# Kernel tuning notes

Hardware: AMD Instinct MI355X
Metric: run time of the kernel (lower is better)

The kernel has to match this reference:

```python
import jax, jax.numpy as jnp
import numpy as np

C_IN, D_STATE, EXPAND, KS = 64, 16, 2, 3
D_INNER = EXPAND * C_IN
HP_KS, HP_SIGMA = 15, 3.0
B, H, W = 4, 256, 256


def _gauss2d(ks, sigma):
    ax = jnp.arange(ks, dtype=jnp.float32) - (ks - 1) / 2.0
    g = jnp.exp(-(ax ** 2) / (2.0 * sigma ** 2))
    g = g / g.sum()
    return jnp.outer(g, g)


def _dwconv(x, w, pad):
    # x: [B,d,H,W], w: [d,1,kh,kw] depthwise
    return jax.lax.conv_general_dilated(
        x, w, window_strides=(1, 1), padding=[(pad, pad), (pad, pad)],
        dimension_numbers=("NCHW", "OIHW", "NCHW"),
        feature_group_count=x.shape[1])


def _selective_scan(u, dt, Bm, Cm, A, D, scan_axis):
    # u, dt: [B,d,H,W]; Bm, Cm: [B,N,H,W]; scan over scan_axis (2 or 3)
    u_s = jnp.moveaxis(u, scan_axis, 0)    # [L,B,d,M]
    dt_s = jnp.moveaxis(dt, scan_axis, 0)
    B_s = jnp.moveaxis(Bm, scan_axis, 0)   # [L,B,N,M]
    C_s = jnp.moveaxis(Cm, scan_axis, 0)
    Bb, d = u.shape[0], u.shape[1]
    M = u_s.shape[-1]
    N = A.shape[1]

    def step(h, inp):
        uj, dtj, Bj, Cj = inp                     # [B,d,M], [B,d,M], [B,N,M], [B,N,M]
        expA = jnp.exp(dtj[..., None] * A[None, :, None, :])   # [B,d,M,N]
        Bt = jnp.transpose(Bj, (0, 2, 1))[:, None]              # [B,1,M,N]
        Ct = jnp.transpose(Cj, (0, 2, 1))[:, None]
        h = expA * h + (uj * dtj)[..., None] * Bt               # [B,d,M,N]
        y = jnp.sum(h * Ct, axis=-1) + D[None, :, None] * uj    # [B,d,M]
        return h, y

    h0 = jnp.zeros((Bb, d, M, N), u.dtype)
    _, ys = jax.lax.scan(step, h0, (u_s, dt_s, B_s, C_s))
    return jnp.moveaxis(ys, 0, scan_axis)


def setup_inputs() -> dict:
    key = jax.random.key(0)
    ks = jax.random.split(key, 12)
    d, N = D_INNER, D_STATE
    A_log = -(jnp.linspace(0.0, 1.0, N, dtype=jnp.float32) * jnp.log(10.0))
    A_log = jnp.broadcast_to(A_log[None, :], (d, N)).astype(jnp.float32)
    return {
        "x": jax.random.normal(ks[0], (B, C_IN, H, W), jnp.float32),
        "in_proj_w": jax.random.normal(ks[1], (2 * d, C_IN), jnp.float32) * 0.05,
        "in_proj_b": jnp.zeros((2 * d,), jnp.float32),
        "dw_w": jax.random.normal(ks[2], (d, 1, KS, KS), jnp.float32) * 0.2,
        "dw_b": jnp.zeros((d,), jnp.float32),
        "xproj_w": jax.random.normal(ks[3], (1 + 2 * N, d), jnp.float32) * 0.05,
        "dtproj_w": jax.random.normal(ks[4], (d, 1), jnp.float32) * 0.5,
        "dtproj_b": jax.random.normal(ks[5], (d,), jnp.float32) * 0.5 - 4.0,
        "A_log": A_log,
        "D": jnp.ones((d,), jnp.float32),
        "out_w": jax.random.normal(ks[6], (C_IN, d), jnp.float32) * 0.05,
        "out_b": jnp.zeros((C_IN,), jnp.float32),
    }


def reference(x, in_proj_w, in_proj_b, dw_w, dw_b, xproj_w,
              dtproj_w, dtproj_b, A_log, D, out_w, out_b):
    d, N = D_INNER, D_STATE
    # in_proj (1x1 conv)
    uz = jnp.einsum("bchw,oc->bohw", x, in_proj_w) + in_proj_b[None, :, None, None]
    U, Z = uz[:, :d], uz[:, d:]
    # depthwise conv
    Uc = _dwconv(U, dw_w, KS // 2) + dw_b[None, :, None, None]
    # tanh(alpha * x) * weight + bias with alpha=0.5, weight=1, bias=0
    Uc = jnp.tanh(0.5 * Uc)
    # Gaussian high-pass: x - depthwise gaussian blur
    g = _gauss2d(HP_KS, HP_SIGMA)
    gk = jnp.broadcast_to(g[None, None], (d, 1, HP_KS, HP_KS))
    Uc = Uc - _dwconv(Uc, gk, HP_KS // 2)
    # x_proj (1x1 conv, no bias)
    params = jnp.einsum("bchw,oc->bohw", Uc, xproj_w)
    delta_in = params[:, :1]                 # [B,1,H,W]
    B_map = params[:, 1:1 + N]               # [B,N,H,W]
    C_map = params[:, 1 + N:1 + 2 * N]
    dt = jax.nn.softplus(jnp.einsum("bohw,do->bdhw", delta_in, dtproj_w)
                         + dtproj_b[None, :, None, None])
    A = -jnp.exp(A_log)
    Y_h = _selective_scan(Uc, dt, B_map, C_map, A, D, scan_axis=3)   # scan over W
    Y_v = _selective_scan(Y_h, dt, B_map, C_map, A, D, scan_axis=2)  # scan over H
    out = Y_v * jax.nn.sigmoid(Z)
    return jnp.einsum("bdhw,cd->bchw", out, out_w) + out_b[None, :, None, None]
```

## Files before the change

kernel.cpp:

```cpp
#include <hip/hip_runtime.h>
#include <hip/hip_bf16.h>
#include <math.h>

#define BB 4
#define CIN 64
#define DI 128
#define NS 16
#define HH 256
#define WW 256
#define HW 65536
#define NCH_P 33

__device__ __forceinline__ float softplusf(float x) {
    return fmaxf(x, 0.f) + __logf(1.0f + __expf(-fabsf(x)));
}
__device__ __forceinline__ float tanh_half(float a) {
    return 1.0f - 2.0f / (1.0f + __expf(a));
}
__device__ __forceinline__ float sigmoidf(float z) {
    return 1.0f / (1.0f + __expf(-z));
}

__device__ __forceinline__ void gauss15(float* g) {
    float s = 0.f;
#pragma unroll
    for (int i = 0; i < 15; ++i) {
        float a = (float)i - 7.0f;
        g[i] = __expf(-a * a / 18.0f);
        s += g[i];
    }
    float inv = 1.0f / s;
#pragma unroll
    for (int i = 0; i < 15; ++i) g[i] *= inv;
}

__global__ __launch_bounds__(256) void k_inproj(
    const float* __restrict__ xb, const float* __restrict__ w,
    const float* __restrict__ bias, float* __restrict__ Ub) {
    int p = blockIdx.x * 256 + threadIdx.x;
    int og = blockIdx.y * 64;
    float xv[CIN];
#pragma unroll
    for (int c = 0; c < CIN; ++c) xv[c] = xb[(size_t)c * HW + p];
#pragma unroll 2
    for (int o = og; o < og + 64; ++o) {
        float a0 = bias[o], a1 = 0.f, a2 = 0.f, a3 = 0.f;
        const float* wr = w + o * CIN;
#pragma unroll
        for (int c = 0; c < CIN; c += 4) {
            a0 = fmaf(xv[c],     wr[c],     a0);
            a1 = fmaf(xv[c + 1], wr[c + 1], a1);
            a2 = fmaf(xv[c + 2], wr[c + 2], a2);
            a3 = fmaf(xv[c + 3], wr[c + 3], a3);
        }
        Ub[(size_t)o * HW + p] = (a0 + a1) + (a2 + a3);
    }
}

#define TILE_H 16
__global__ __launch_bounds__(256) void k_conv(
    const float* __restrict__ Ub, const float* __restrict__ dww,
    const float* __restrict__ dwb, float* __restrict__ Ucb) {
    __shared__ float sU[32 * 256];
    __shared__ float sC[30 * 272];
    int c  = blockIdx.x >> 4;
    int t  = blockIdx.x & 15;
    int h0 = t * TILE_H;
    int w  = threadIdx.x;

    const float* base = Ub + (size_t)c * HW;
#pragma unroll
    for (int i = 0; i < 32; ++i) {
        int hh = h0 + i - 8;
        sU[i * 256 + w] = (hh >= 0 && hh < HH) ? base[hh * WW + w] : 0.f;
    }
    __syncthreads();

    float wt[9];
#pragma unroll
    for (int i = 0; i < 9; ++i) wt[i] = dww[c * 9 + i];
    float bb = dwb[c];

#pragma unroll
    for (int i = 0; i < 30; ++i) {
        int r = h0 + i - 7;
        float v = 0.f;
        if (r >= 0 && r < HH) {
            float acc = bb;
#pragma unroll
            for (int ky = 0; ky < 3; ++ky) {
                const float* ur = sU + (i + ky) * 256;
#pragma unroll
                for (int kx = 0; kx < 3; ++kx) {
                    int ww = w + kx - 1;
                    if (ww >= 0 && ww < WW) acc = fmaf(ur[ww], wt[ky * 3 + kx], acc);
                }
            }
            v = tanh_half(acc);
        }
        sC[i * 272 + w + 7] = v;
    }
    if (w < 7) {
#pragma unroll
        for (int i = 0; i < 30; ++i) { sC[i * 272 + w] = 0.f; sC[i * 272 + w + 263] = 0.f; }
    }
    __syncthreads();

    float g[15]; gauss15(g);
#pragma unroll
    for (int i = 0; i < 30; ++i) {
        float acc = 0.f;
#pragma unroll
        for (int k = 0; k < 15; ++k) acc = fmaf(sC[i * 272 + w + k], g[k], acc);
        sU[i * 256 + w] = acc;
    }
    float* outp = Ucb + (size_t)c * HW + h0 * WW + w;
#pragma unroll
    for (int i = 0; i < TILE_H; ++i) {
        float acc = 0.f;
#pragma unroll
        for (int k = 0; k < 15; ++k) acc = fmaf(sU[(i + k) * 256 + w], g[k], acc);
        float center = sC[(i + 7) * 272 + w + 7];
        outp[i * WW] = center - acc;
    }
}

__global__ __launch_bounds__(256) void k_xproj(
    const float* __restrict__ Uc, const float* __restrict__ xw,
    float* __restrict__ P) {
    int p = blockIdx.x * 256 + threadIdx.x;
    int b = p >> 16;
    int rem = p & 65535;
    const float* up = Uc + (size_t)b * DI * HW + rem;
    float acc[NCH_P];
#pragma unroll
    for (int o = 0; o < NCH_P; ++o) acc[o] = 0.f;
    for (int c = 0; c < DI; ++c) {
        float u = up[(size_t)c * HW];
#pragma unroll
        for (int o = 0; o < NCH_P; ++o) acc[o] = fmaf(u, xw[o * DI + c], acc[o]);
    }
    float* pp = P + (size_t)b * NCH_P * HW + rem;
#pragma unroll
    for (int o = 0; o < NCH_P; ++o) pp[(size_t)o * HW] = acc[o];
}

#define CW 32
__global__ __launch_bounds__(128) void k_scan_w(
    float* __restrict__ UY, const float* __restrict__ P,
    const float* __restrict__ A_log, const float* __restrict__ dtw,
    const float* __restrict__ dtb, const float* __restrict__ Dv) {
    __shared__ float sU[DI * 33];
    __shared__ float sP[CW * 36];
    int bh = blockIdx.x;
    int b = bh >> 8;
    int h = bh & 255;
    int t = threadIdx.x;

    float Av[NS];
#pragma unroll
    for (int n = 0; n < NS; ++n) Av[n] = -__expf(A_log[t * NS + n]);
    float wdt = dtw[t], bdt = dtb[t], Dd = Dv[t];
    float hS[NS];
#pragma unroll
    for (int n = 0; n < NS; ++n) hS[n] = 0.f;

    float* ubase = UY + (size_t)(b * DI) * HW + (size_t)h * WW;
    const float* prow = P + (size_t)(b * NCH_P) * HW + (size_t)h * WW;

    const int w4 = (t & 7) * 4;
    const int dbase = t >> 3;

    float4 rU[8];
    float rP[9];
#pragma unroll
    for (int p = 0; p < 8; ++p)
        rU[p] = *(const float4*)(ubase + (size_t)(dbase + p * 16) * HW + w4);
#pragma unroll
    for (int i = 0; i < 9; ++i) {
        int idx = i * 128 + t, ch = idx >> 5, wi = idx & 31;
        rP[i] = (ch < NCH_P) ? prow[(size_t)ch * HW + wi] : 0.f;
    }

    for (int w0 = 0; w0 < WW; w0 += CW) {
#pragma unroll
        for (int p = 0; p < 8; ++p) {
            float* s = sU + (dbase + p * 16) * 33 + w4;
            s[0] = rU[p].x; s[1] = rU[p].y; s[2] = rU[p].z; s[3] = rU[p].w;
        }
#pragma unroll
        for (int i = 0; i < 9; ++i) {
            int idx = i * 128 + t, ch = idx >> 5, wi = idx & 31;
            if (ch < NCH_P) sP[wi * 36 + ch] = rP[i];
        }
        __syncthreads();
        if (w0 + CW < WW) {
#pragma unroll
            for (int p = 0; p < 8; ++p)
                rU[p] = *(const float4*)(ubase + (size_t)(dbase + p * 16) * HW + w0 + CW + w4);
#pragma unroll
            for (int i = 0; i < 9; ++i) {
                int idx = i * 128 + t, ch = idx >> 5, wi = idx & 31;
                rP[i] = (ch < NCH_P) ? prow[(size_t)ch * HW + w0 + CW + wi] : 0.f;
            }
        }
#pragma unroll 2
        for (int wi = 0; wi < CW; ++wi) {
            const float* pr = sP + wi * 36;
            float4 q0 = *(const float4*)(pr);
            float4 q1 = *(const float4*)(pr + 4);
            float4 q2 = *(const float4*)(pr + 8);
            float4 q3 = *(const float4*)(pr + 12);
            float4 q4 = *(const float4*)(pr + 16);
            float4 q5 = *(const float4*)(pr + 20);
            float4 q6 = *(const float4*)(pr + 24);
            float4 q7 = *(const float4*)(pr + 28);
            float q8 = pr[32];
            float u = sU[t * 33 + wi];
            float dt = softplusf(fmaf(q0.x, wdt, bdt));
            float ud = u * dt;
            float y = Dd * u;
            float Bv[NS] = {q0.y,q0.z,q0.w,q1.x,q1.y,q1.z,q1.w,q2.x,
                            q2.y,q2.z,q2.w,q3.x,q3.y,q3.z,q3.w,q4.x};
            float Cv[NS] = {q4.y,q4.z,q4.w,q5.x,q5.y,q5.z,q5.w,q6.x,
                            q6.y,q6.z,q6.w,q7.x,q7.y,q7.z,q7.w,q8};
#pragma unroll
            for (int n = 0; n < NS; ++n) {
                float e = __expf(dt * Av[n]);
                hS[n] = fmaf(e, hS[n], ud * Bv[n]);
                y = fmaf(hS[n], Cv[n], y);
            }
            sU[t * 33 + wi] = y;
        }
        __syncthreads();
#pragma unroll
        for (int p = 0; p < 8; ++p) {
            const float* s = sU + (dbase + p * 16) * 33 + w4;
            float4 v; v.x = s[0]; v.y = s[1]; v.z = s[2]; v.w = s[3];
            *(float4*)(ubase + (size_t)(dbase + p * 16) * HW + w0 + w4) = v;
        }
        __syncthreads();
    }
}

#define PF_U(uu, hp_) { int hp = (hp_); if (hp > HH - 1) hp = HH - 1; \
    uu = ub[hp * WW + w]; }
#define PF_P(dde, Bp, Cp, hp_) { int hp = (hp_); if (hp > HH - 1) hp = HH - 1; \
    int off = hp * WW + w; dde = pb[off]; \
    _Pragma("unroll") for (int n = 0; n < NS; ++n) { \
        Bp[n] = pb[(1 + n) * HW + off]; Cp[n] = pb[(17 + n) * HW + off]; } }
#define ROW(hh, uu, dde, Bp, Cp) { \
    float dt = softplusf(fmaf(dde, wdt, bdt)); \
    float ud = uu * dt; \
    float y = Dd * uu; \
    _Pragma("unroll") for (int n = 0; n < NS; ++n) { \
        float e = __expf(dt * Av[n]); \
        hS[n] = fmaf(e, hS[n], ud * Bp[n]); \
        y = fmaf(hS[n], Cp[n], y); } \
    ub[(hh) * WW + w] = y; }

__global__ __launch_bounds__(256) void k_scan_h(
    float* __restrict__ UY, const float* __restrict__ P,
    const float* __restrict__ A_log, const float* __restrict__ dtw,
    const float* __restrict__ dtb, const float* __restrict__ Dv) {
    int bd = blockIdx.x;
    int b = bd >> 7;
    int d = bd & (DI - 1);
    int w = threadIdx.x;
    float Av[NS];
#pragma unroll
    for (int n = 0; n < NS; ++n) Av[n] = -__expf(A_log[d * NS + n]);
    float wdt = dtw[d], bdt = dtb[d], Dd = Dv[d];
    float* ub = UY + (size_t)bd * HW;
    const float* pb = P + (size_t)b * NCH_P * HW;
    float hS[NS];
#pragma unroll
    for (int n = 0; n < NS; ++n) hS[n] = 0.f;

    float u0, u1, u2, u3;
    float deA, deB;
    float BA[NS], CA[NS], Bb[NS], Cb[NS];

    PF_U(u0, 0); PF_U(u1, 1); PF_U(u2, 2); PF_U(u3, 3);
    PF_P(deA, BA, CA, 0);
    PF_P(deB, Bb, Cb, 1);

#pragma unroll 1
    for (int h = 0; h < HH; h += 4) {
        ROW(h,     u0, deA, BA, CA);  PF_P(deA, BA, CA, h + 2);  PF_U(u0, h + 4);
        ROW(h + 1, u1, deB, Bb, Cb);  PF_P(deB, Bb, Cb, h + 3);  PF_U(u1, h + 5);
        ROW(h + 2, u2, deA, BA, CA);  PF_P(deA, BA, CA, h + 4);  PF_U(u2, h + 6);
        ROW(h + 3, u3, deB, Bb, Cb);  PF_P(deB, Bb, Cb, h + 5);  PF_U(u3, h + 7);
    }
}

__global__ __launch_bounds__(256) void k_gate(
    float* __restrict__ Y, const float* __restrict__ x,
    const float* __restrict__ wz, const float* __restrict__ bz) {
    int p = blockIdx.x * 256 + threadIdx.x;
    int b = p >> 16;
    int rem = p & 65535;
    const float* xp = x + (size_t)b * CIN * HW + rem;
    float xv[CIN];
#pragma unroll
    for (int c = 0; c < CIN; ++c) xv[c] = xp[(size_t)c * HW];
    float* yp = Y + (size_t)b * DI * HW + rem;
#pragma unroll 2
    for (int dd = 0; dd < DI; ++dd) {
        float z0 = 0.f, z1 = 0.f, z2 = 0.f, z3 = 0.f;
        const float* wr = wz + dd * CIN;
#pragma unroll
        for (int c = 0; c < CIN; c += 4) {
            z0 = fmaf(xv[c],     wr[c],     z0);
            z1 = fmaf(xv[c + 1], wr[c + 1], z1);
            z2 = fmaf(xv[c + 2], wr[c + 2], z2);
            z3 = fmaf(xv[c + 3], wr[c + 3], z3);
        }
        float z = bz[dd] + ((z0 + z1) + (z2 + z3));
        float yv = yp[(size_t)dd * HW];
        yp[(size_t)dd * HW] = yv * sigmoidf(z);
    }
}

__global__ __launch_bounds__(256) void k_out2(
    const float* __restrict__ G, const float* __restrict__ ow,
    const float* __restrict__ ob, float* __restrict__ outp) {
    int p = blockIdx.x * 256 + threadIdx.x;
    int b = p >> 16;
    int rem = p & 65535;
    const float* gp = G + (size_t)b * DI * HW + rem;
    float acc[CIN];
#pragma unroll
    for (int c = 0; c < CIN; ++c) acc[c] = 0.f;
    for (int dd = 0; dd < DI; ++dd) {
        float g = gp[(size_t)dd * HW];
#pragma unroll
        for (int c = 0; c < CIN; ++c) acc[c] = fmaf(g, ow[c * DI + dd], acc[c]);
    }
    float* op = outp + (size_t)b * CIN * HW + rem;
#pragma unroll
    for (int c = 0; c < CIN; ++c) op[(size_t)c * HW] = acc[c] + ob[c];
}

extern "C" void kernel_launch(void* const* d_in, const int* in_sizes, int n_in,
                              void* d_out, int out_size, void* d_ws, size_t ws_size,
                              hipStream_t stream) {
    const float* x     = (const float*)d_in[0];
    const float* ipw   = (const float*)d_in[1];
    const float* ipb   = (const float*)d_in[2];
    const float* dww   = (const float*)d_in[3];
    const float* dwb   = (const float*)d_in[4];
    const float* xpw   = (const float*)d_in[5];
    const float* dtw   = (const float*)d_in[6];
    const float* dtb   = (const float*)d_in[7];
    const float* A_log = (const float*)d_in[8];
    const float* Dv    = (const float*)d_in[9];
    const float* ow    = (const float*)d_in[10];
    const float* ob    = (const float*)d_in[11];
    float* out = (float*)d_out;

    const float* wz = ipw + (size_t)DI * CIN;
    const float* bz = ipb + DI;

    const size_t PLANE = (size_t)DI * HW;
    const size_t NB    = (size_t)BB * PLANE;

    if (ws_size >= (NB + PLANE) * sizeof(float)) {
        float* bufY = (float*)d_ws;
        float* bufU = bufY + NB;
        float* P    = out;
        for (int b = 0; b < BB; ++b) {
            k_inproj<<<dim3(HW / 256, 2), 256, 0, stream>>>(x + (size_t)b * CIN * HW, ipw, ipb, bufU);
            k_conv<<<DI * 16, 256, 0, stream>>>(bufU, dww, dwb, bufY + (size_t)b * PLANE);
        }
        k_xproj<<<BB * (HW / 256), 256, 0, stream>>>(bufY, xpw, P);
        k_scan_w<<<BB * HH, 128, 0, stream>>>(bufY, P, A_log, dtw, dtb, Dv);
        k_scan_h<<<BB * DI, 256, 0, stream>>>(bufY, P, A_log, dtw, dtb, Dv);
        k_gate<<<BB * (HW / 256), 256, 0, stream>>>(bufY, x, wz, bz);
        k_out2<<<BB * (HW / 256), 256, 0, stream>>>(bufY, ow, ob, out);
    } else {
        float* bufA = (float*)d_ws;
        float* bufY = bufA + PLANE;
        for (int b = 0; b < BB; ++b) {
            const float* xb = x + (size_t)b * CIN * HW;
            k_inproj<<<dim3(HW / 256, 2), 256, 0, stream>>>(xb, ipw, ipb, bufA);
            k_conv<<<DI * 16, 256, 0, stream>>>(bufA, dww, dwb, bufY);
            k_xproj<<<HW / 256, 256, 0, stream>>>(bufY, xpw, bufA);
            k_scan_w<<<HH, 128, 0, stream>>>(bufY, bufA, A_log, dtw, dtb, Dv);
            k_scan_h<<<DI, 256, 0, stream>>>(bufY, bufA, A_log, dtw, dtb, Dv);
            k_gate<<<HW / 256, 256, 0, stream>>>(bufY, xb, wz, bz);
            k_out2<<<HW / 256, 256, 0, stream>>>(bufY, ow, ob, out + (size_t)b * CIN * HW);
        }
    }
}
```

Before: 1.496 ms.

## Store x_proj outputs pixel-interleaved to vectorize scan parameter loads

The x_proj output (delta, B, C) moves from a channel-planar layout to a pixel-major layout padded to 36 floats per pixel. k_xproj stages its results through shared memory so the writes go out as coalesced float4 stores. Both scan kernels then fetch each pixel's parameters with float4 loads instead of 33 separate strided scalar loads. The padding adds about a tenth more parameter traffic, and k_scan_h's per-thread loads now stride 144 bytes apart, though each warp's accesses together still span one contiguous region.

```diff
diff --git a/kernel.cpp b/kernel.cpp
--- a/kernel.cpp
+++ b/kernel.cpp
@@ -10,6 +10,7 @@
 #define WW 256
 #define HW 65536
 #define NCH_P 33
+#define PT_STRIDE 36
 
 __device__ __forceinline__ float softplusf(float x) {
     return fmaxf(x, 0.f) + __logf(1.0f + __expf(-fabsf(x)));
@@ -127,8 +128,11 @@
 
 __global__ __launch_bounds__(256) void k_xproj(
     const float* __restrict__ Uc, const float* __restrict__ xw,
-    float* __restrict__ P) {
-    int p = blockIdx.x * 256 + threadIdx.x;
+    float* __restrict__ Pt) {
+    __shared__ float4 sT4[2304];
+    float* sT = (float*)sT4;
+    int t = threadIdx.x;
+    int p = blockIdx.x * 256 + t;
     int b = p >> 16;
     int rem = p & 65535;
     const float* up = Uc + (size_t)b * DI * HW + rem;
@@ -140,18 +144,23 @@
 #pragma unroll
         for (int o = 0; o < NCH_P; ++o) acc[o] = fmaf(u, xw[o * DI + c], acc[o]);
     }
-    float* pp = P + (size_t)b * NCH_P * HW + rem;
-#pragma unroll
-    for (int o = 0; o < NCH_P; ++o) pp[(size_t)o * HW] = acc[o];
+#pragma unroll
+    for (int o = 0; o < NCH_P; ++o) sT[t * PT_STRIDE + o] = acc[o];
+    __syncthreads();
+    int rem0 = (blockIdx.x * 256) & 65535;
+    float4* dst = (float4*)(Pt + ((size_t)b * HW + (size_t)rem0) * PT_STRIDE);
+#pragma unroll
+    for (int k = 0; k < 9; ++k) dst[k * 256 + t] = sT4[k * 256 + t];
 }
 
 #define CW 32
 __global__ __launch_bounds__(128) void k_scan_w(
-    float* __restrict__ UY, const float* __restrict__ P,
+    float* __restrict__ UY, const float* __restrict__ Pt,
     const float* __restrict__ A_log, const float* __restrict__ dtw,
     const float* __restrict__ dtb, const float* __restrict__ Dv) {
     __shared__ float sU[DI * 33];
-    __shared__ float sP[CW * 36];
+    __shared__ float4 sP4[288];
+    float* sP = (float*)sP4;
     int bh = blockIdx.x;
     int b = bh >> 8;
     int h = bh & 255;
@@ -166,20 +175,20 @@
     for (int n = 0; n < NS; ++n) hS[n] = 0.f;
 
     float* ubase = UY + (size_t)(b * DI) * HW + (size_t)h * WW;
-    const float* prow = P + (size_t)(b * NCH_P) * HW + (size_t)h * WW;
+    const float4* ptrow = (const float4*)(Pt + ((size_t)b * HW + (size_t)h * WW) * PT_STRIDE);
 
     const int w4 = (t & 7) * 4;
     const int dbase = t >> 3;
 
     float4 rU[8];
-    float rP[9];
+    float4 rT[3];
 #pragma unroll
     for (int p = 0; p < 8; ++p)
         rU[p] = *(const float4*)(ubase + (size_t)(dbase + p * 16) * HW + w4);
 #pragma unroll
-    for (int i = 0; i < 9; ++i) {
-        int idx = i * 128 + t, ch = idx >> 5, wi = idx & 31;
-        rP[i] = (ch < NCH_P) ? prow[(size_t)ch * HW + wi] : 0.f;
+    for (int k = 0; k < 3; ++k) {
+        int idx = k * 128 + t;
+        if (idx < 288) rT[k] = ptrow[idx];
     }
 
     for (int w0 = 0; w0 < WW; w0 += CW) {
@@ -189,9 +198,9 @@
             s[0] = rU[p].x; s[1] = rU[p].y; s[2] = rU[p].z; s[3] = rU[p].w;
         }
 #pragma unroll
-        for (int i = 0; i < 9; ++i) {
-            int idx = i * 128 + t, ch = idx >> 5, wi = idx & 31;
-            if (ch < NCH_P) sP[wi * 36 + ch] = rP[i];
+        for (int k = 0; k < 3; ++k) {
+            int idx = k * 128 + t;
+            if (idx < 288) sP4[idx] = rT[k];
         }
         __syncthreads();
         if (w0 + CW < WW) {
@@ -199,14 +208,14 @@
             for (int p = 0; p < 8; ++p)
                 rU[p] = *(const float4*)(ubase + (size_t)(dbase + p * 16) * HW + w0 + CW + w4);
 #pragma unroll
-            for (int i = 0; i < 9; ++i) {
-                int idx = i * 128 + t, ch = idx >> 5, wi = idx & 31;
-                rP[i] = (ch < NCH_P) ? prow[(size_t)ch * HW + w0 + CW + wi] : 0.f;
+            for (int k = 0; k < 3; ++k) {
+                int idx = k * 128 + t;
+                if (idx < 288) rT[k] = ptrow[(w0 + CW) * 9 + idx];
             }
         }
 #pragma unroll 2
         for (int wi = 0; wi < CW; ++wi) {
-            const float* pr = sP + wi * 36;
+            const float* pr = sP + wi * PT_STRIDE;
             float4 q0 = *(const float4*)(pr);
             float4 q1 = *(const float4*)(pr + 4);
             float4 q2 = *(const float4*)(pr + 8);
@@ -245,22 +254,26 @@
 
 #define PF_U(uu, hp_) { int hp = (hp_); if (hp > HH - 1) hp = HH - 1; \
     uu = ub[hp * WW + w]; }
-#define PF_P(dde, Bp, Cp, hp_) { int hp = (hp_); if (hp > HH - 1) hp = HH - 1; \
-    int off = hp * WW + w; dde = pb[off]; \
-    _Pragma("unroll") for (int n = 0; n < NS; ++n) { \
-        Bp[n] = pb[(1 + n) * HW + off]; Cp[n] = pb[(17 + n) * HW + off]; } }
-#define ROW(hh, uu, dde, Bp, Cp) { \
-    float dt = softplusf(fmaf(dde, wdt, bdt)); \
+#define PF_PT(q, q8, hp_) { int hp = (hp_); if (hp > HH - 1) hp = HH - 1; \
+    const float* pr = pbt + (hp * WW + w) * PT_STRIDE; \
+    _Pragma("unroll") for (int i = 0; i < 8; ++i) q[i] = *(const float4*)(pr + i * 4); \
+    q8 = pr[32]; }
+#define ROWT(hh, uu, q, q8) { \
+    float dt = softplusf(fmaf(q[0].x, wdt, bdt)); \
     float ud = uu * dt; \
     float y = Dd * uu; \
+    float Bv[NS] = {q[0].y,q[0].z,q[0].w,q[1].x,q[1].y,q[1].z,q[1].w,q[2].x, \
+                    q[2].y,q[2].z,q[2].w,q[3].x,q[3].y,q[3].z,q[3].w,q[4].x}; \
+    float Cv[NS] = {q[4].y,q[4].z,q[4].w,q[5].x,q[5].y,q[5].z,q[5].w,q[6].x, \
+                    q[6].y,q[6].z,q[6].w,q[7].x,q[7].y,q[7].z,q[7].w,q8}; \
     _Pragma("unroll") for (int n = 0; n < NS; ++n) { \
         float e = __expf(dt * Av[n]); \
-        hS[n] = fmaf(e, hS[n], ud * Bp[n]); \
-        y = fmaf(hS[n], Cp[n], y); } \
+        hS[n] = fmaf(e, hS[n], ud * Bv[n]); \
+        y = fmaf(hS[n], Cv[n], y); } \
     ub[(hh) * WW + w] = y; }
 
 __global__ __launch_bounds__(256) void k_scan_h(
-    float* __restrict__ UY, const float* __restrict__ P,
+    float* __restrict__ UY, const float* __restrict__ Pt,
     const float* __restrict__ A_log, const float* __restrict__ dtw,
     const float* __restrict__ dtb, const float* __restrict__ Dv) {
     int bd = blockIdx.x;
@@ -272,25 +285,25 @@
     for (int n = 0; n < NS; ++n) Av[n] = -__expf(A_log[d * NS + n]);
     float wdt = dtw[d], bdt = dtb[d], Dd = Dv[d];
     float* ub = UY + (size_t)bd * HW;
-    const float* pb = P + (size_t)b * NCH_P * HW;
+    const float* pbt = Pt + (size_t)b * HW * PT_STRIDE;
     float hS[NS];
 #pragma unroll
     for (int n = 0; n < NS; ++n) hS[n] = 0.f;
 
     float u0, u1, u2, u3;
-    float deA, deB;
-    float BA[NS], CA[NS], Bb[NS], Cb[NS];
+    float4 qA[8]; float qA8;
+    float4 qB[8]; float qB8;
 
     PF_U(u0, 0); PF_U(u1, 1); PF_U(u2, 2); PF_U(u3, 3);
-    PF_P(deA, BA, CA, 0);
-    PF_P(deB, Bb, Cb, 1);
+    PF_PT(qA, qA8, 0);
+    PF_PT(qB, qB8, 1);
 
 #pragma unroll 1
     for (int h = 0; h < HH; h += 4) {
-        ROW(h,     u0, deA, BA, CA);  PF_P(deA, BA, CA, h + 2);  PF_U(u0, h + 4);
-        ROW(h + 1, u1, deB, Bb, Cb);  PF_P(deB, Bb, Cb, h + 3);  PF_U(u1, h + 5);
-        ROW(h + 2, u2, deA, BA, CA);  PF_P(deA, BA, CA, h + 4);  PF_U(u2, h + 6);
-        ROW(h + 3, u3, deB, Bb, Cb);  PF_P(deB, Bb, Cb, h + 5);  PF_U(u3, h + 7);
+        ROWT(h,     u0, qA, qA8);  PF_PT(qA, qA8, h + 2);  PF_U(u0, h + 4);
+        ROWT(h + 1, u1, qB, qB8);  PF_PT(qB, qB8, h + 3);  PF_U(u1, h + 5);
+        ROWT(h + 2, u2, qA, qA8);  PF_PT(qA, qA8, h + 4);  PF_U(u2, h + 6);
+        ROWT(h + 3, u3, qB, qB8);  PF_PT(qB, qB8, h + 5);  PF_U(u3, h + 7);
     }
 }
 
@@ -368,14 +381,14 @@
     if (ws_size >= (NB + PLANE) * sizeof(float)) {
         float* bufY = (float*)d_ws;
         float* bufU = bufY + NB;
-        float* P    = out;
+        float* Pt   = out;
         for (int b = 0; b < BB; ++b) {
             k_inproj<<<dim3(HW / 256, 2), 256, 0, stream>>>(x + (size_t)b * CIN * HW, ipw, ipb, bufU);
             k_conv<<<DI * 16, 256, 0, stream>>>(bufU, dww, dwb, bufY + (size_t)b * PLANE);
         }
-        k_xproj<<<BB * (HW / 256), 256, 0, stream>>>(bufY, xpw, P);
-        k_scan_w<<<BB * HH, 128, 0, stream>>>(bufY, P, A_log, dtw, dtb, Dv);
-        k_scan_h<<<BB * DI, 256, 0, stream>>>(bufY, P, A_log, dtw, dtb, Dv);
+        k_xproj<<<BB * (HW / 256), 256, 0, stream>>>(bufY, xpw, Pt);
+        k_scan_w<<<BB * HH, 128, 0, stream>>>(bufY, Pt, A_log, dtw, dtb, Dv);
+        k_scan_h<<<BB * DI, 256, 0, stream>>>(bufY, Pt, A_log, dtw, dtb, Dv);
         k_gate<<<BB * (HW / 256), 256, 0, stream>>>(bufY, x, wz, bz);
         k_out2<<<BB * (HW / 256), 256, 0, stream>>>(bufY, ow, ob, out);
     } else {
```

Result: slower. 1.826 ms (+22.1%).

## Share B/C/delta parameter rows across four channels via double-buffered LDS in H-scan

Applied to the files above, without the earlier changes.

The vertical scan kernel now gives each block 4 channels by 64 columns instead of one channel by all 256 columns. Threads load the 33 parameter channels for two rows cooperatively into a double-buffered LDS tile, so each parameter value is fetched from global memory once per 4 channels instead of once per channel. Rows are pipelined with register prefetch and barriers. This cuts global traffic on P and register pressure from the 64-float prefetch arrays, at the cost of two barriers per pair of rows and LDS reads in the inner loop.

```diff
diff --git a/kernel.cpp b/kernel.cpp
--- a/kernel.cpp
+++ b/kernel.cpp
@@ -243,54 +243,82 @@
     }
 }
 
-#define PF_U(uu, hp_) { int hp = (hp_); if (hp > HH - 1) hp = HH - 1; \
-    uu = ub[hp * WW + w]; }
-#define PF_P(dde, Bp, Cp, hp_) { int hp = (hp_); if (hp > HH - 1) hp = HH - 1; \
-    int off = hp * WW + w; dde = pb[off]; \
-    _Pragma("unroll") for (int n = 0; n < NS; ++n) { \
-        Bp[n] = pb[(1 + n) * HW + off]; Cp[n] = pb[(17 + n) * HW + off]; } }
-#define ROW(hh, uu, dde, Bp, Cp) { \
-    float dt = softplusf(fmaf(dde, wdt, bdt)); \
-    float ud = uu * dt; \
-    float y = Dd * uu; \
+#define WT2 64
+
+#define LD2(hb) { \
+    _Pragma("unroll") for (int rr = 0; rr < 2; ++rr) { \
+        int hp = (hb) + rr; if (hp > HH - 1) hp = HH - 1; \
+        const float* pr_ = pt + hp * WW; \
+        _Pragma("unroll") for (int k = 0; k < 8; ++k) rp[rr][k] = pr_[(size_t)(4 * k) * HW]; \
+        rp8[rr] = (dl == 0) ? pr_[(size_t)32 * HW] : 0.f; \
+    } }
+#define WR2(bf) { \
+    _Pragma("unroll") for (int rr = 0; rr < 2; ++rr) { \
+        _Pragma("unroll") for (int k = 0; k < 8; ++k) sP[bf][rr][4 * k + dl][wl] = rp[rr][k]; \
+        if (dl == 0) sP[bf][rr][32][wl] = rp8[rr]; \
+    } }
+#define PU2(uu, hp_) { int hp = (hp_); if (hp > HH - 1) hp = HH - 1; uu = ub[hp * WW]; }
+#define CP2(bf, rr, hh, uu) { \
+    const float* pr_ = &sP[bf][rr][0][wl]; \
+    float de = pr_[0]; \
+    float dt = softplusf(fmaf(de, wdt, bdt)); \
+    float ud = (uu) * dt; \
+    float y = Dd * (uu); \
     _Pragma("unroll") for (int n = 0; n < NS; ++n) { \
         float e = __expf(dt * Av[n]); \
-        hS[n] = fmaf(e, hS[n], ud * Bp[n]); \
-        y = fmaf(hS[n], Cp[n], y); } \
-    ub[(hh) * WW + w] = y; }
+        hS[n] = fmaf(e, hS[n], ud * pr_[(1 + n) * WT2]); \
+        y = fmaf(hS[n], pr_[(17 + n) * WT2], y); } \
+    ub[(hh) * WW] = y; }
 
 __global__ __launch_bounds__(256) void k_scan_h(
     float* __restrict__ UY, const float* __restrict__ P,
     const float* __restrict__ A_log, const float* __restrict__ dtw,
     const float* __restrict__ dtb, const float* __restrict__ Dv) {
-    int bd = blockIdx.x;
-    int b = bd >> 7;
-    int d = bd & (DI - 1);
-    int w = threadIdx.x;
+    __shared__ float sP[2][2][NCH_P][WT2];
+    int bid = blockIdx.x;
+    int b  = bid >> 7;
+    int r  = bid & 127;
+    int wt = r >> 5;
+    int dg = r & 31;
+    int t  = threadIdx.x;
+    int dl = t >> 6;
+    int wl = t & 63;
+    int d  = dg * 4 + dl;
+
     float Av[NS];
 #pragma unroll
     for (int n = 0; n < NS; ++n) Av[n] = -__expf(A_log[d * NS + n]);
     float wdt = dtw[d], bdt = dtb[d], Dd = Dv[d];
-    float* ub = UY + (size_t)bd * HW;
-    const float* pb = P + (size_t)b * NCH_P * HW;
     float hS[NS];
 #pragma unroll
     for (int n = 0; n < NS; ++n) hS[n] = 0.f;
 
-    float u0, u1, u2, u3;
-    float deA, deB;
-    float BA[NS], CA[NS], Bb[NS], Cb[NS];
-
-    PF_U(u0, 0); PF_U(u1, 1); PF_U(u2, 2); PF_U(u3, 3);
-    PF_P(deA, BA, CA, 0);
-    PF_P(deB, Bb, Cb, 1);
+    float* ub = UY + (size_t)(b * DI + d) * HW + wt * WT2 + wl;
+    const float* pt = P + (size_t)b * NCH_P * HW + (size_t)dl * HW + wt * WT2 + wl;
+
+    float rp[2][8], rp8[2];
+    float uA0, uA1, uB0, uB1;
+
+    LD2(0);
+    PU2(uA0, 0); PU2(uA1, 1); PU2(uB0, 2); PU2(uB1, 3);
+    WR2(0);
+    __syncthreads();
+    LD2(2);
 
 #pragma unroll 1
-    for (int h = 0; h < HH; h += 4) {
-        ROW(h,     u0, deA, BA, CA);  PF_P(deA, BA, CA, h + 2);  PF_U(u0, h + 4);
-        ROW(h + 1, u1, deB, Bb, Cb);  PF_P(deB, Bb, Cb, h + 3);  PF_U(u1, h + 5);
-        ROW(h + 2, u2, deA, BA, CA);  PF_P(deA, BA, CA, h + 4);  PF_U(u2, h + 6);
-        ROW(h + 3, u3, deB, Bb, Cb);  PF_P(deB, Bb, Cb, h + 5);  PF_U(u3, h + 7);
+    for (int h0 = 0; h0 < HH; h0 += 4) {
+        CP2(0, 0, h0,     uA0);
+        CP2(0, 1, h0 + 1, uA1);
+        WR2(1);
+        __syncthreads();
+        LD2(h0 + 4);
+        PU2(uA0, h0 + 4); PU2(uA1, h0 + 5);
+        CP2(1, 0, h0 + 2, uB0);
+        CP2(1, 1, h0 + 3, uB1);
+        WR2(0);
+        __syncthreads();
+        LD2(h0 + 6);
+        PU2(uB0, h0 + 6); PU2(uB1, h0 + 7);
     }
 }
 
@@ -375,7 +403,7 @@
         }
         k_xproj<<<BB * (HW / 256), 256, 0, stream>>>(bufY, xpw, P);
         k_scan_w<<<BB * HH, 128, 0, stream>>>(bufY, P, A_log, dtw, dtb, Dv);
-        k_scan_h<<<BB * DI, 256, 0, stream>>>(bufY, P, A_log, dtw, dtb, Dv);
+        k_scan_h<<<BB * 128, 256, 0, stream>>>(bufY, P, A_log, dtw, dtb, Dv);
         k_gate<<<BB * (HW / 256), 256, 0, stream>>>(bufY, x, wz, bz);
         k_out2<<<BB * (HW / 256), 256, 0, stream>>>(bufY, ow, ob, out);
     } else {
@@ -387,7 +415,7 @@
             k_conv<<<DI * 16, 256, 0, stream>>>(bufA, dww, dwb, bufY);
             k_xproj<<<HW / 256, 256, 0, stream>>>(bufY, xpw, bufA);
             k_scan_w<<<HH, 128, 0, stream>>>(bufY, bufA, A_log, dtw, dtb, Dv);
-            k_scan_h<<<DI, 256, 0, stream>>>(bufY, bufA, A_log, dtw, dtb, Dv);
+            k_scan_h<<<128, 256, 0, stream>>>(bufY, bufA, A_log, dtw, dtb, Dv);
             k_gate<<<HW / 256, 256, 0, stream>>>(bufY, xb, wz, bz);
             k_out2<<<HW / 256, 256, 0, stream>>>(bufY, ow, ob, out + (size_t)b * CIN * HW);
         }
```

After: 1.463 ms. 1.02x faster.
